# Optimization experiments

Measured on AMD Instinct MI355X. Metric: run time of the kernel, lower is better.

The kernel has to match this reference:

```python
import jax, jax.numpy as jnp
import numpy as np

B, S, DIM = 2, 1024, 1024
E, K, INTER = 16, 2, 512
SHARED_INTER = 2 * INTER  # n_shared_experts * moe_inter_dim
ROUTE_SCALE = 1.0


def setup_inputs() -> dict:
    key = jax.random.key(0)
    ks = jax.random.split(key, 8)
    init = lambda k, shape: jax.random.normal(k, shape, dtype=jnp.float32) * 0.02
    return {
        "x": jax.random.normal(ks[0], (B, S, DIM), dtype=jnp.float32),
        "gate_w": init(ks[1], (E, DIM)),
        "w1": init(ks[2], (E, INTER, DIM)),
        "w2": init(ks[3], (E, DIM, INTER)),
        "w3": init(ks[4], (E, INTER, DIM)),
        "sw1": init(ks[5], (SHARED_INTER, DIM)),
        "sw2": init(ks[6], (DIM, SHARED_INTER)),
        "sw3": init(ks[7], (SHARED_INTER, DIM)),
    }


def reference(x, gate_w, w1, w2, w3, sw1, sw2, sw3):
    b, s, d = x.shape
    xt = x.reshape(-1, d)            # [T, D] flattened tokens
    T = xt.shape[0]

    # Gate: sigmoid scores, top-k experts, normalize selected weights
    scores = jax.nn.sigmoid(xt @ gate_w.T)           # [T, E]
    topv, topi = jax.lax.top_k(scores, K)            # [T, K]
    weights = topv / jnp.sum(topv, axis=-1, keepdims=True) * ROUTE_SCALE

    # Per-token dense combine weights over experts: gate[t, e]
    gate = jnp.zeros((T, E), xt.dtype).at[jnp.arange(T)[:, None], topi].add(weights)

    # Routed experts (SwiGLU), computed densely and combined with gate weights
    h = jax.nn.silu(jnp.einsum('td,eid->tei', xt, w1)) * jnp.einsum('td,eid->tei', xt, w3)
    expert_out = jnp.einsum('tei,edi->ted', h, w2)   # [T, E, D]
    y = jnp.einsum('ted,te->td', expert_out, gate)   # [T, D]

    # Shared expert (SwiGLU MLP over all tokens)
    z = (jax.nn.silu(xt @ sw1.T) * (xt @ sw3.T)) @ sw2.T

    return (y + z).reshape(b, s, d)
```

## Files before the change

kernel.cpp:

```cpp
#include <hip/hip_runtime.h>
#include <stdint.h>

typedef unsigned short u16;
typedef __bf16 bf16x8 __attribute__((ext_vector_type(8)));
typedef float f32x4 __attribute__((ext_vector_type(4)));
typedef unsigned short u16x8 __attribute__((ext_vector_type(8)));

#define TTOK 2048
#define DIMSZ 1024
#define NROUT 16
#define INTERSZ 512
#define BK 128
#define CHK 16

__device__ __forceinline__ u16 f2bf(float f) {
    unsigned int u = __builtin_bit_cast(unsigned int, f);
    unsigned int r = u + 0x7FFFu + ((u >> 16) & 1u);
    return (u16)(r >> 16);
}

__device__ __forceinline__ void gl2lds16(const void* g, void* l) {
    __builtin_amdgcn_global_load_lds(
        (const __attribute__((address_space(1))) void*)(uintptr_t)g,
        (__attribute__((address_space(3))) void*)(uintptr_t)l,
        16, 0, 0);
}

#define NF4A (NROUT * INTERSZ * DIMSZ / 4)
#define NF4B (DIMSZ * DIMSZ / 4)
#define CASTA_BLKS 1024
#define CAST_BLKS 1152
__global__ __launch_bounds__(256) void prep(
    const float* __restrict__ w1, const float* __restrict__ sw1,
    const float* __restrict__ w3, const float* __restrict__ sw3,
    const float* __restrict__ w2, const float* __restrict__ sw2,
    u16* __restrict__ W1b, u16* __restrict__ W3b, u16* __restrict__ W2b,
    const float* __restrict__ x, const float* __restrict__ gw,
    int* __restrict__ topi, float2* __restrict__ topw,
    u16* __restrict__ Xbf) {
    const int r = blockIdx.y;
    const int tid = threadIdx.x;
    if (r < 3) {
        if (blockIdx.x >= CAST_BLKS) return;
        const float* a; const float* b; u16* d;
        if (r == 0)      { a = w1; b = sw1; d = W1b; }
        else if (r == 1) { a = w3; b = sw3; d = W3b; }
        else             { a = w2; b = sw2; d = W2b; }
        const float4* src = (blockIdx.x < CASTA_BLKS)
                            ? (const float4*)a
                            : (const float4*)b - (size_t)CASTA_BLKS * 2048;
        ushort4* dst = (ushort4*)d;
        const size_t gbase = (size_t)blockIdx.x * 2048;
        float4 v[8];
        #pragma unroll
        for (int k = 0; k < 8; ++k)
            v[k] = src[gbase + k * 256 + tid];
        #pragma unroll
        for (int k = 0; k < 8; ++k) {
            ushort4 o;
            o.x = f2bf(v[k].x); o.y = f2bf(v[k].y);
            o.z = f2bf(v[k].z); o.w = f2bf(v[k].w);
            dst[gbase + k * 256 + tid] = o;
        }
        return;
    }
    const int t = blockIdx.x;
    const int wave = tid >> 6, lane = tid & 63;
    const int d0 = tid * 4;
    float4 xv = *(const float4*)(x + (size_t)t * DIMSZ + d0);
    ushort4 o;
    o.x = f2bf(xv.x); o.y = f2bf(xv.y); o.z = f2bf(xv.z); o.w = f2bf(xv.w);
    *(ushort4*)&Xbf[(size_t)t * DIMSZ + d0] = o;

    float acc[16];
    #pragma unroll
    for (int e = 0; e < 16; ++e) {
        float4 g = *(const float4*)(gw + e * DIMSZ + d0);
        acc[e] = xv.x * g.x + xv.y * g.y + xv.z * g.z + xv.w * g.w;
    }
    #pragma unroll
    for (int off = 32; off > 0; off >>= 1) {
        #pragma unroll
        for (int e = 0; e < 16; ++e) acc[e] += __shfl_xor(acc[e], off);
    }
    __shared__ float part[4][16];
    __shared__ float sfin[16];
    if (lane < 16) part[wave][lane] = acc[lane];
    __syncthreads();
    if (wave == 0 && lane < 16) {
        float s = part[0][lane] + part[1][lane] + part[2][lane] + part[3][lane];
        sfin[lane] = 1.f / (1.f + expf(-s));
    }
    __syncthreads();
    if (tid == 0) {
        int i0 = 0; float v0 = sfin[0];
        #pragma unroll
        for (int e = 1; e < 16; ++e) { float v = sfin[e]; if (v > v0) { v0 = v; i0 = e; } }
        int i1 = -1; float v1 = -1e30f;
        #pragma unroll
        for (int e = 0; e < 16; ++e) { float v = sfin[e]; if (e != i0 && v > v1) { v1 = v; i1 = e; } }
        float inv = 1.f / (v0 + v1);
        topi[t] = i0 | (i1 << 8);
        topw[t] = make_float2(v0 * inv, v1 * inv);
    }
}

__global__ __launch_bounds__(256) void route_kernel(
    const int* __restrict__ topi, const float2* __restrict__ topw,
    int* __restrict__ counts, int* __restrict__ tokidx, float* __restrict__ tokw) {
    const int e = blockIdx.x;
    const int tid = threadIdx.x;
    int p[8]; int m[8]; int cnt = 0;
    #pragma unroll
    for (int j = 0; j < 8; ++j) {
        int t = tid * 8 + j;
        p[j] = topi[t];
        m[j] = ((p[j] & 255) == e) || ((p[j] >> 8) == e) ? 1 : 0;
        cnt += m[j];
    }
    const int lane = tid & 63, wave = tid >> 6;
    int v = cnt;
    #pragma unroll
    for (int off = 1; off < 64; off <<= 1) {
        int u = __shfl_up(v, off);
        if (lane >= off) v += u;
    }
    __shared__ int wsum[4];
    if (lane == 63) wsum[wave] = v;
    __syncthreads();
    int wbase = 0;
    #pragma unroll
    for (int w = 0; w < 4; ++w) wbase += (w < wave) ? wsum[w] : 0;
    int base = wbase + v - cnt;
    #pragma unroll
    for (int j = 0; j < 8; ++j) {
        if (m[j]) {
            int t = tid * 8 + j;
            float2 w2 = topw[t];
            tokidx[e * TTOK + base] = t;
            tokw[e * TTOK + base] = ((p[j] & 255) == e) ? w2.x : w2.y;
            ++base;
        }
    }
    if (tid == 0) counts[e] = wsum[0] + wsum[1] + wsum[2] + wsum[3];
}

__global__ __launch_bounds__(256) void gemm1s(
    const u16* __restrict__ Xbf, const u16* __restrict__ W1b,
    const u16* __restrict__ W3b, const int* __restrict__ counts,
    const int* __restrict__ tokidx, const float* __restrict__ tokw,
    u16* __restrict__ Hc, u16* __restrict__ Hs) {
    const int e = blockIdx.z;
    const int cnt = (e < NROUT) ? counts[e] : TTOK;
    const int m0 = blockIdx.y * 64;
    if (m0 >= cnt) return;
    const int n0 = blockIdx.x * 64;
    __shared__ u16 As[64 * BK], B1s[64 * BK], B3s[64 * BK];
    const u16* B1 = W1b + ((size_t)e * INTERSZ + n0) * DIMSZ;
    const u16* B3 = W3b + ((size_t)e * INTERSZ + n0) * DIMSZ;
    const int tid = threadIdx.x;

    int row[4], cgs[4]; size_t arow[4];
    #pragma unroll
    for (int i = 0; i < 4; ++i) {
        int c = tid + i * 256;
        row[i] = c >> 4;
        cgs[i] = ((c & 15) ^ (row[i] & 7)) * 8;
        int slot = m0 + row[i];
        int g;
        if (e < NROUT) g = (slot < cnt) ? tokidx[e * TTOK + slot] : 0;
        else           g = slot;
        arow[i] = (size_t)g * DIMSZ;
    }
    f32x4 acc1[2][2] = {}; f32x4 acc3[2][2] = {};
    const int wave = tid >> 6, lane = tid & 63;
    const int wm = (wave >> 1) * 32, wn = (wave & 1) * 32;
    const int lr = lane & 15, lq = lane >> 4;

    for (int kt = 0; kt < DIMSZ / BK; ++kt) {
        const int k0 = kt * BK;
        #pragma unroll
        for (int i = 0; i < 4; ++i) {
            int c = tid + i * 256;
            gl2lds16(Xbf + arow[i] + k0 + cgs[i], &As[c * 8]);
            size_t boff = (size_t)row[i] * DIMSZ + k0 + cgs[i];
            gl2lds16(B1 + boff, &B1s[c * 8]);
            gl2lds16(B3 + boff, &B3s[c * 8]);
        }
        __syncthreads();
        #pragma unroll
        for (int ks = 0; ks < 4; ++ks) {
            bf16x8 af[2], b1f[2], b3f[2];
            const int g = ks * 4 + lq;
            #pragma unroll
            for (int mt = 0; mt < 2; ++mt) {
                int m = wm + mt * 16 + lr;
                af[mt] = *(const bf16x8*)&As[(m * CHK + (g ^ (m & 7))) * 8];
            }
            #pragma unroll
            for (int nt = 0; nt < 2; ++nt) {
                int n = wn + nt * 16 + lr;
                int ch = (n * CHK + (g ^ (n & 7))) * 8;
                b1f[nt] = *(const bf16x8*)&B1s[ch];
                b3f[nt] = *(const bf16x8*)&B3s[ch];
            }
            #pragma unroll
            for (int mt = 0; mt < 2; ++mt) {
                #pragma unroll
                for (int nt = 0; nt < 2; ++nt) {
                    acc1[mt][nt] = __builtin_amdgcn_mfma_f32_16x16x32_bf16(af[mt], b1f[nt], acc1[mt][nt], 0, 0, 0);
                    acc3[mt][nt] = __builtin_amdgcn_mfma_f32_16x16x32_bf16(af[mt], b3f[nt], acc3[mt][nt], 0, 0, 0);
                }
            }
        }
        __syncthreads();
    }
    #pragma unroll
    for (int mt = 0; mt < 2; ++mt) {
        #pragma unroll
        for (int nt = 0; nt < 2; ++nt) {
            #pragma unroll
            for (int r = 0; r < 4; ++r) {
                int m = wm + mt * 16 + lq * 4 + r;
                int n = wn + nt * 16 + lr;
                int slot = m0 + m;
                bool valid = slot < cnt;
                float h1 = acc1[mt][nt][r], h3 = acc3[mt][nt][r];
                float hv = 0.f;
                if (valid) {
                    float tw = (e < NROUT) ? tokw[e * TTOK + slot] : 1.0f;
                    hv = h1 / (1.f + __expf(-h1)) * h3 * tw;
                }
                if (e < NROUT)
                    Hc[((size_t)e * TTOK + slot) * INTERSZ + n0 + n] = f2bf(hv);
                else
                    Hs[(size_t)slot * DIMSZ + (e - NROUT) * INTERSZ + n0 + n] = f2bf(hv);
            }
        }
    }
}

__global__ __launch_bounds__(256) void gemm2rt(
    const u16* __restrict__ Hc, const u16* __restrict__ W2b,
    const int* __restrict__ counts, const int* __restrict__ tokidx,
    const int* __restrict__ topi,
    float* __restrict__ bufA, float* __restrict__ bufB) {
    const int e = blockIdx.z;
    const int cnt = counts[e];
    const int m0 = blockIdx.y * 64;
    if (m0 >= cnt) return;
    const int n0 = blockIdx.x * 64;
    __shared__ u16 As[64 * BK], Bs[64 * BK];
    const u16* A0 = Hc + ((size_t)e * TTOK + m0) * INTERSZ;
    const u16* B0 = W2b + ((size_t)e * DIMSZ + n0) * INTERSZ;
    const int tid = threadIdx.x;
    const int wave = tid >> 6, lane = tid & 63;
    const int wm = (wave >> 1) * 32, wn = (wave & 1) * 32;
    const int lr = lane & 15, lq = lane >> 4;

    int row[4], cgs[4];
    #pragma unroll
    for (int i = 0; i < 4; ++i) {
        int c = tid + i * 256;
        row[i] = c >> 4;
        cgs[i] = ((c & 15) ^ (row[i] & 7)) * 8;
    }

    f32x4 acc[2][2] = {};
    for (int kt = 0; kt < INTERSZ / BK; ++kt) {
        const int k0 = kt * BK;
        #pragma unroll
        for (int i = 0; i < 4; ++i) {
            int c = tid + i * 256;
            gl2lds16(A0 + (size_t)row[i] * INTERSZ + k0 + cgs[i], &As[c * 8]);
            gl2lds16(B0 + (size_t)row[i] * INTERSZ + k0 + cgs[i], &Bs[c * 8]);
        }
        __syncthreads();
        #pragma unroll
        for (int ks = 0; ks < 4; ++ks) {
            bf16x8 af[2], bfr[2];
            const int g = ks * 4 + lq;
            #pragma unroll
            for (int mt = 0; mt < 2; ++mt) {
                int m = wm + mt * 16 + lr;
                af[mt] = *(const bf16x8*)&As[(m * CHK + (g ^ (m & 7))) * 8];
            }
            #pragma unroll
            for (int nt = 0; nt < 2; ++nt) {
                int n = wn + nt * 16 + lr;
                bfr[nt] = *(const bf16x8*)&Bs[(n * CHK + (g ^ (n & 7))) * 8];
            }
            #pragma unroll
            for (int mt = 0; mt < 2; ++mt) {
                #pragma unroll
                for (int nt = 0; nt < 2; ++nt) {
                    acc[mt][nt] = __builtin_amdgcn_mfma_f32_16x16x32_bf16(af[mt], bfr[nt], acc[mt][nt], 0, 0, 0);
                }
            }
        }
        __syncthreads();
    }
    #pragma unroll
    for (int mt = 0; mt < 2; ++mt) {
        #pragma unroll
        for (int r = 0; r < 4; ++r) {
            int m = wm + mt * 16 + lq * 4 + r;
            int slot = m0 + m;
            if (slot < cnt) {
                int t = tokidx[e * TTOK + slot];
                float* db = ((topi[t] & 255) == e) ? bufA : bufB;
                #pragma unroll
                for (int nt = 0; nt < 2; ++nt) {
                    int n = wn + nt * 16 + lr;
                    db[(size_t)t * DIMSZ + n0 + n] = acc[mt][nt][r];
                }
            }
        }
    }
}

__global__ __launch_bounds__(256) void gemm2sh(
    const u16* __restrict__ Hs, const u16* __restrict__ W2sb,
    const float* __restrict__ bufA, const float* __restrict__ bufB,
    float* __restrict__ out) {
    const int m0 = blockIdx.y * 64;
    const int n0 = blockIdx.x * 64;
    __shared__ u16 As[64 * BK], Bs[64 * BK];
    const u16* A0 = Hs + (size_t)m0 * DIMSZ;
    const u16* B0 = W2sb + (size_t)n0 * DIMSZ;
    const int tid = threadIdx.x;
    const int wave = tid >> 6, lane = tid & 63;
    const int wm = (wave >> 1) * 32, wn = (wave & 1) * 32;
    const int lr = lane & 15, lq = lane >> 4;

    int row[4], cgs[4];
    #pragma unroll
    for (int i = 0; i < 4; ++i) {
        int c = tid + i * 256;
        row[i] = c >> 4;
        cgs[i] = ((c & 15) ^ (row[i] & 7)) * 8;
    }

    f32x4 acc[2][2] = {};
    for (int kt = 0; kt < DIMSZ / BK; ++kt) {
        const int k0 = kt * BK;
        #pragma unroll
        for (int i = 0; i < 4; ++i) {
            int c = tid + i * 256;
            gl2lds16(A0 + (size_t)row[i] * DIMSZ + k0 + cgs[i], &As[c * 8]);
            gl2lds16(B0 + (size_t)row[i] * DIMSZ + k0 + cgs[i], &Bs[c * 8]);
        }
        __syncthreads();
        #pragma unroll
        for (int ks = 0; ks < 4; ++ks) {
            bf16x8 af[2], bfr[2];
            const int g = ks * 4 + lq;
            #pragma unroll
            for (int mt = 0; mt < 2; ++mt) {
                int m = wm + mt * 16 + lr;
                af[mt] = *(const bf16x8*)&As[(m * CHK + (g ^ (m & 7))) * 8];
            }
            #pragma unroll
            for (int nt = 0; nt < 2; ++nt) {
                int n = wn + nt * 16 + lr;
                bfr[nt] = *(const bf16x8*)&Bs[(n * CHK + (g ^ (n & 7))) * 8];
            }
            #pragma unroll
            for (int mt = 0; mt < 2; ++mt) {
                #pragma unroll
                for (int nt = 0; nt < 2; ++nt) {
                    acc[mt][nt] = __builtin_amdgcn_mfma_f32_16x16x32_bf16(af[mt], bfr[nt], acc[mt][nt], 0, 0, 0);
                }
            }
        }
        __syncthreads();
    }
    #pragma unroll
    for (int mt = 0; mt < 2; ++mt) {
        #pragma unroll
        for (int r = 0; r < 4; ++r) {
            int t = m0 + wm + mt * 16 + lq * 4 + r;
            #pragma unroll
            for (int nt = 0; nt < 2; ++nt) {
                int n = wn + nt * 16 + lr;
                size_t idx = (size_t)t * DIMSZ + n0 + n;
                out[idx] = acc[mt][nt][r] + bufA[idx] + bufB[idx];
            }
        }
    }
}

extern "C" void kernel_launch(void* const* d_in, const int* in_sizes, int n_in,
                              void* d_out, int out_size, void* d_ws, size_t ws_size,
                              hipStream_t stream) {
    const float* x      = (const float*)d_in[0];
    const float* gate_w = (const float*)d_in[1];
    const float* w1     = (const float*)d_in[2];
    const float* w2     = (const float*)d_in[3];
    const float* w3     = (const float*)d_in[4];
    const float* sw1    = (const float*)d_in[5];
    const float* sw2    = (const float*)d_in[6];
    const float* sw3    = (const float*)d_in[7];
    float* out = (float*)d_out;

    char* ws = (char*)d_ws;
    const size_t SZ_W   = (size_t)(NROUT + 2) * INTERSZ * DIMSZ * 2;
    const size_t SZ_XBF = (size_t)TTOK * DIMSZ * 2;
    u16*   W1b    = (u16*)(ws);
    u16*   W3b    = (u16*)(ws + SZ_W);
    u16*   W2all  = (u16*)(ws + 2 * SZ_W);
    u16*   Xbf    = (u16*)(ws + 3 * SZ_W);
    char*  route  = ws + 3 * SZ_W + SZ_XBF;
    int*   counts = (int*)route;
    int*   topi   = (int*)(route + 256);
    float2* topw  = (float2*)(route + 256 + TTOK * 4);
    int*   tokidx = (int*)(route + 256 + TTOK * 12);
    float* tokw   = (float*)(route + 256 + TTOK * 12 + 16 * TTOK * 4);
    char*  hbuf   = route + 256 + TTOK * 12 + 2 * (size_t)16 * TTOK * 4;
    u16*   Hc     = (u16*)hbuf;
    u16*   Hs     = (u16*)(hbuf + (size_t)NROUT * TTOK * INTERSZ * 2);
    char*  bufs   = hbuf + (size_t)NROUT * TTOK * INTERSZ * 2 + (size_t)TTOK * DIMSZ * 2;
    float* bufA   = (float*)bufs;
    float* bufB   = (float*)(bufs + (size_t)TTOK * DIMSZ * 4);
    u16*   W2sb   = W2all + (size_t)NROUT * DIMSZ * INTERSZ;

    prep<<<dim3(2048, 4), 256, 0, stream>>>(
        w1, sw1, w3, sw3, w2, sw2, W1b, W3b, W2all,
        x, gate_w, topi, topw, Xbf);
    route_kernel<<<NROUT, 256, 0, stream>>>(topi, topw, counts, tokidx, tokw);
    gemm1s<<<dim3(INTERSZ / 64, TTOK / 64, NROUT + 2), 256, 0, stream>>>(
        Xbf, W1b, W3b, counts, tokidx, tokw, Hc, Hs);
    gemm2rt<<<dim3(DIMSZ / 64, TTOK / 64, NROUT), 256, 0, stream>>>(
        Hc, W2all, counts, tokidx, topi, bufA, bufB);
    gemm2sh<<<dim3(DIMSZ / 64, TTOK / 64), 256, 0, stream>>>(
        Hs, W2sb, bufA, bufB, out);
}
```

Baseline: 230.8 us.

## Double-buffer LDS tiles in all GEMMs with BK 64 and split prep kernel

All three GEMM kernels now use BK=64 with two LDS buffers. The next K-tile is fetched by direct global-to-LDS loads while the current tile runs through MFMA, and a single wait plus barrier per iteration replaces the two syncthreads. s_setprio is raised during the MFMA section. The combined prep kernel is split into a weight-cast kernel and a gate/X-cast kernel, which removes the idle blocks of the old 2D grid. The risks are more loop iterations and barriers, and dependence on the loads in flight covering the compute of each iteration.

```diff
diff --git a/kernel.cpp b/kernel.cpp
--- a/kernel.cpp
+++ b/kernel.cpp
@@ -10,8 +10,8 @@
 #define DIMSZ 1024
 #define NROUT 16
 #define INTERSZ 512
-#define BK 128
-#define CHK 16
+#define BK 64
+#define CHK 8
 
 __device__ __forceinline__ u16 f2bf(float f) {
     unsigned int u = __builtin_bit_cast(unsigned int, f);
@@ -27,43 +27,41 @@
 }
 
 #define NF4A (NROUT * INTERSZ * DIMSZ / 4)
-#define NF4B (DIMSZ * DIMSZ / 4)
 #define CASTA_BLKS 1024
-#define CAST_BLKS 1152
-__global__ __launch_bounds__(256) void prep(
+__global__ __launch_bounds__(256) void prep_cast(
     const float* __restrict__ w1, const float* __restrict__ sw1,
     const float* __restrict__ w3, const float* __restrict__ sw3,
     const float* __restrict__ w2, const float* __restrict__ sw2,
-    u16* __restrict__ W1b, u16* __restrict__ W3b, u16* __restrict__ W2b,
+    u16* __restrict__ W1b, u16* __restrict__ W3b, u16* __restrict__ W2b) {
+    const int r = blockIdx.y;
+    const int tid = threadIdx.x;
+    const float* a; const float* b; u16* d;
+    if (r == 0)      { a = w1; b = sw1; d = W1b; }
+    else if (r == 1) { a = w3; b = sw3; d = W3b; }
+    else             { a = w2; b = sw2; d = W2b; }
+    const float4* src = (blockIdx.x < CASTA_BLKS)
+                        ? (const float4*)a
+                        : (const float4*)b - (size_t)CASTA_BLKS * 2048;
+    ushort4* dst = (ushort4*)d;
+    const size_t gbase = (size_t)blockIdx.x * 2048;
+    float4 v[8];
+    #pragma unroll
+    for (int k = 0; k < 8; ++k)
+        v[k] = src[gbase + k * 256 + tid];
+    #pragma unroll
+    for (int k = 0; k < 8; ++k) {
+        ushort4 o;
+        o.x = f2bf(v[k].x); o.y = f2bf(v[k].y);
+        o.z = f2bf(v[k].z); o.w = f2bf(v[k].w);
+        dst[gbase + k * 256 + tid] = o;
+    }
+}
+
+__global__ __launch_bounds__(256) void prep_gate(
     const float* __restrict__ x, const float* __restrict__ gw,
     int* __restrict__ topi, float2* __restrict__ topw,
     u16* __restrict__ Xbf) {
-    const int r = blockIdx.y;
-    const int tid = threadIdx.x;
-    if (r < 3) {
-        if (blockIdx.x >= CAST_BLKS) return;
-        const float* a; const float* b; u16* d;
-        if (r == 0)      { a = w1; b = sw1; d = W1b; }
-        else if (r == 1) { a = w3; b = sw3; d = W3b; }
-        else             { a = w2; b = sw2; d = W2b; }
-        const float4* src = (blockIdx.x < CASTA_BLKS)
-                            ? (const float4*)a
-                            : (const float4*)b - (size_t)CASTA_BLKS * 2048;
-        ushort4* dst = (ushort4*)d;
-        const size_t gbase = (size_t)blockIdx.x * 2048;
-        float4 v[8];
-        #pragma unroll
-        for (int k = 0; k < 8; ++k)
-            v[k] = src[gbase + k * 256 + tid];
-        #pragma unroll
-        for (int k = 0; k < 8; ++k) {
-            ushort4 o;
-            o.x = f2bf(v[k].x); o.y = f2bf(v[k].y);
-            o.z = f2bf(v[k].z); o.w = f2bf(v[k].w);
-            dst[gbase + k * 256 + tid] = o;
-        }
-        return;
-    }
+    const int tid = threadIdx.x;
     const int t = blockIdx.x;
     const int wave = tid >> 6, lane = tid & 63;
     const int d0 = tid * 4;
@@ -155,17 +153,17 @@
     const int m0 = blockIdx.y * 64;
     if (m0 >= cnt) return;
     const int n0 = blockIdx.x * 64;
-    __shared__ u16 As[64 * BK], B1s[64 * BK], B3s[64 * BK];
+    __shared__ u16 As[2][64 * BK], B1s[2][64 * BK], B3s[2][64 * BK];
     const u16* B1 = W1b + ((size_t)e * INTERSZ + n0) * DIMSZ;
     const u16* B3 = W3b + ((size_t)e * INTERSZ + n0) * DIMSZ;
     const int tid = threadIdx.x;
 
-    int row[4], cgs[4]; size_t arow[4];
-    #pragma unroll
-    for (int i = 0; i < 4; ++i) {
+    int row[2], cgs[2]; size_t arow[2];
+    #pragma unroll
+    for (int i = 0; i < 2; ++i) {
         int c = tid + i * 256;
-        row[i] = c >> 4;
-        cgs[i] = ((c & 15) ^ (row[i] & 7)) * 8;
+        row[i] = c >> 3;
+        cgs[i] = ((c & 7) ^ (row[i] & 7)) * 8;
         int slot = m0 + row[i];
         int g;
         if (e < NROUT) g = (slot < cnt) ? tokidx[e * TTOK + slot] : 0;
@@ -176,33 +174,43 @@
     const int wave = tid >> 6, lane = tid & 63;
     const int wm = (wave >> 1) * 32, wn = (wave & 1) * 32;
     const int lr = lane & 15, lq = lane >> 4;
-
-    for (int kt = 0; kt < DIMSZ / BK; ++kt) {
-        const int k0 = kt * BK;
-        #pragma unroll
-        for (int i = 0; i < 4; ++i) {
-            int c = tid + i * 256;
-            gl2lds16(Xbf + arow[i] + k0 + cgs[i], &As[c * 8]);
-            size_t boff = (size_t)row[i] * DIMSZ + k0 + cgs[i];
-            gl2lds16(B1 + boff, &B1s[c * 8]);
-            gl2lds16(B3 + boff, &B3s[c * 8]);
-        }
-        __syncthreads();
-        #pragma unroll
-        for (int ks = 0; ks < 4; ++ks) {
+    const int NKT = DIMSZ / BK;
+
+#define STG1(kt, h) { \
+    const int k0_ = (kt) * BK; \
+    _Pragma("unroll") \
+    for (int i = 0; i < 2; ++i) { \
+        int c = tid + i * 256; \
+        gl2lds16(Xbf + arow[i] + k0_ + cgs[i], &As[h][c * 8]); \
+        size_t boff = (size_t)row[i] * DIMSZ + k0_ + cgs[i]; \
+        gl2lds16(B1 + boff, &B1s[h][c * 8]); \
+        gl2lds16(B3 + boff, &B3s[h][c * 8]); \
+    } }
+
+    STG1(0, 0);
+    asm volatile("s_waitcnt vmcnt(0)" ::: "memory");
+    __builtin_amdgcn_s_barrier();
+
+    #pragma unroll 2
+    for (int kt = 0; kt < NKT; ++kt) {
+        const int cur = kt & 1;
+        if (kt + 1 < NKT) STG1(kt + 1, cur ^ 1);
+        __builtin_amdgcn_s_setprio(1);
+        #pragma unroll
+        for (int ks = 0; ks < 2; ++ks) {
             bf16x8 af[2], b1f[2], b3f[2];
             const int g = ks * 4 + lq;
             #pragma unroll
             for (int mt = 0; mt < 2; ++mt) {
                 int m = wm + mt * 16 + lr;
-                af[mt] = *(const bf16x8*)&As[(m * CHK + (g ^ (m & 7))) * 8];
+                af[mt] = *(const bf16x8*)&As[cur][(m * CHK + (g ^ (m & 7))) * 8];
             }
             #pragma unroll
             for (int nt = 0; nt < 2; ++nt) {
                 int n = wn + nt * 16 + lr;
                 int ch = (n * CHK + (g ^ (n & 7))) * 8;
-                b1f[nt] = *(const bf16x8*)&B1s[ch];
-                b3f[nt] = *(const bf16x8*)&B3s[ch];
+                b1f[nt] = *(const bf16x8*)&B1s[cur][ch];
+                b3f[nt] = *(const bf16x8*)&B3s[cur][ch];
             }
             #pragma unroll
             for (int mt = 0; mt < 2; ++mt) {
@@ -213,8 +221,11 @@
                 }
             }
         }
-        __syncthreads();
-    }
+        __builtin_amdgcn_s_setprio(0);
+        asm volatile("s_waitcnt vmcnt(0)" ::: "memory");
+        __builtin_amdgcn_s_barrier();
+    }
+#undef STG1
     #pragma unroll
     for (int mt = 0; mt < 2; ++mt) {
         #pragma unroll
@@ -250,7 +261,7 @@
     const int m0 = blockIdx.y * 64;
     if (m0 >= cnt) return;
     const int n0 = blockIdx.x * 64;
-    __shared__ u16 As[64 * BK], Bs[64 * BK];
+    __shared__ u16 As[2][64 * BK], Bs[2][64 * BK];
     const u16* A0 = Hc + ((size_t)e * TTOK + m0) * INTERSZ;
     const u16* B0 = W2b + ((size_t)e * DIMSZ + n0) * INTERSZ;
     const int tid = threadIdx.x;
@@ -258,37 +269,47 @@
     const int wm = (wave >> 1) * 32, wn = (wave & 1) * 32;
     const int lr = lane & 15, lq = lane >> 4;
 
-    int row[4], cgs[4];
-    #pragma unroll
-    for (int i = 0; i < 4; ++i) {
+    int row[2], cgs[2];
+    #pragma unroll
+    for (int i = 0; i < 2; ++i) {
         int c = tid + i * 256;
-        row[i] = c >> 4;
-        cgs[i] = ((c & 15) ^ (row[i] & 7)) * 8;
-    }
-
+        row[i] = c >> 3;
+        cgs[i] = ((c & 7) ^ (row[i] & 7)) * 8;
+    }
     f32x4 acc[2][2] = {};
-    for (int kt = 0; kt < INTERSZ / BK; ++kt) {
-        const int k0 = kt * BK;
-        #pragma unroll
-        for (int i = 0; i < 4; ++i) {
-            int c = tid + i * 256;
-            gl2lds16(A0 + (size_t)row[i] * INTERSZ + k0 + cgs[i], &As[c * 8]);
-            gl2lds16(B0 + (size_t)row[i] * INTERSZ + k0 + cgs[i], &Bs[c * 8]);
-        }
-        __syncthreads();
-        #pragma unroll
-        for (int ks = 0; ks < 4; ++ks) {
+    const int NKT = INTERSZ / BK;
+
+#define STG2(kt, h) { \
+    const int k0_ = (kt) * BK; \
+    _Pragma("unroll") \
+    for (int i = 0; i < 2; ++i) { \
+        int c = tid + i * 256; \
+        gl2lds16(A0 + (size_t)row[i] * INTERSZ + k0_ + cgs[i], &As[h][c * 8]); \
+        gl2lds16(B0 + (size_t)row[i] * INTERSZ + k0_ + cgs[i], &Bs[h][c * 8]); \
+    } }
+
+    STG2(0, 0);
+    asm volatile("s_waitcnt vmcnt(0)" ::: "memory");
+    __builtin_amdgcn_s_barrier();
+
+    #pragma unroll 2
+    for (int kt = 0; kt < NKT; ++kt) {
+        const int cur = kt & 1;
+        if (kt + 1 < NKT) STG2(kt + 1, cur ^ 1);
+        __builtin_amdgcn_s_setprio(1);
+        #pragma unroll
+        for (int ks = 0; ks < 2; ++ks) {
             bf16x8 af[2], bfr[2];
             const int g = ks * 4 + lq;
             #pragma unroll
             for (int mt = 0; mt < 2; ++mt) {
                 int m = wm + mt * 16 + lr;
-                af[mt] = *(const bf16x8*)&As[(m * CHK + (g ^ (m & 7))) * 8];
+                af[mt] = *(const bf16x8*)&As[cur][(m * CHK + (g ^ (m & 7))) * 8];
             }
             #pragma unroll
             for (int nt = 0; nt < 2; ++nt) {
                 int n = wn + nt * 16 + lr;
-                bfr[nt] = *(const bf16x8*)&Bs[(n * CHK + (g ^ (n & 7))) * 8];
+                bfr[nt] = *(const bf16x8*)&Bs[cur][(n * CHK + (g ^ (n & 7))) * 8];
             }
             #pragma unroll
             for (int mt = 0; mt < 2; ++mt) {
@@ -298,8 +319,11 @@
                 }
             }
         }
-        __syncthreads();
-    }
+        __builtin_amdgcn_s_setprio(0);
+        asm volatile("s_waitcnt vmcnt(0)" ::: "memory");
+        __builtin_amdgcn_s_barrier();
+    }
+#undef STG2
     #pragma unroll
     for (int mt = 0; mt < 2; ++mt) {
         #pragma unroll
@@ -325,7 +349,7 @@
     float* __restrict__ out) {
     const int m0 = blockIdx.y * 64;
     const int n0 = blockIdx.x * 64;
-    __shared__ u16 As[64 * BK], Bs[64 * BK];
+    __shared__ u16 As[2][64 * BK], Bs[2][64 * BK];
     const u16* A0 = Hs + (size_t)m0 * DIMSZ;
     const u16* B0 = W2sb + (size_t)n0 * DIMSZ;
     const int tid = threadIdx.x;
@@ -333,37 +357,47 @@
     const int wm = (wave >> 1) * 32, wn = (wave & 1) * 32;
     const int lr = lane & 15, lq = lane >> 4;
 
-    int row[4], cgs[4];
-    #pragma unroll
-    for (int i = 0; i < 4; ++i) {
+    int row[2], cgs[2];
+    #pragma unroll
+    for (int i = 0; i < 2; ++i) {
         int c = tid + i * 256;
-        row[i] = c >> 4;
-        cgs[i] = ((c & 15) ^ (row[i] & 7)) * 8;
-    }
-
+        row[i] = c >> 3;
+        cgs[i] = ((c & 7) ^ (row[i] & 7)) * 8;
+    }
     f32x4 acc[2][2] = {};
-    for (int kt = 0; kt < DIMSZ / BK; ++kt) {
-        const int k0 = kt * BK;
-        #pragma unroll
-        for (int i = 0; i < 4; ++i) {
-            int c = tid + i * 256;
-            gl2lds16(A0 + (size_t)row[i] * DIMSZ + k0 + cgs[i], &As[c * 8]);
-            gl2lds16(B0 + (size_t)row[i] * DIMSZ + k0 + cgs[i], &Bs[c * 8]);
-        }
-        __syncthreads();
-        #pragma unroll
-        for (int ks = 0; ks < 4; ++ks) {
+    const int NKT = DIMSZ / BK;
+
+#define STG3(kt, h) { \
+    const int k0_ = (kt) * BK; \
+    _Pragma("unroll") \
+    for (int i = 0; i < 2; ++i) { \
+        int c = tid + i * 256; \
+        gl2lds16(A0 + (size_t)row[i] * DIMSZ + k0_ + cgs[i], &As[h][c * 8]); \
+        gl2lds16(B0 + (size_t)row[i] * DIMSZ + k0_ + cgs[i], &Bs[h][c * 8]); \
+    } }
+
+    STG3(0, 0);
+    asm volatile("s_waitcnt vmcnt(0)" ::: "memory");
+    __builtin_amdgcn_s_barrier();
+
+    #pragma unroll 2
+    for (int kt = 0; kt < NKT; ++kt) {
+        const int cur = kt & 1;
+        if (kt + 1 < NKT) STG3(kt + 1, cur ^ 1);
+        __builtin_amdgcn_s_setprio(1);
+        #pragma unroll
+        for (int ks = 0; ks < 2; ++ks) {
             bf16x8 af[2], bfr[2];
             const int g = ks * 4 + lq;
             #pragma unroll
             for (int mt = 0; mt < 2; ++mt) {
                 int m = wm + mt * 16 + lr;
-                af[mt] = *(const bf16x8*)&As[(m * CHK + (g ^ (m & 7))) * 8];
+                af[mt] = *(const bf16x8*)&As[cur][(m * CHK + (g ^ (m & 7))) * 8];
             }
             #pragma unroll
             for (int nt = 0; nt < 2; ++nt) {
                 int n = wn + nt * 16 + lr;
-                bfr[nt] = *(const bf16x8*)&Bs[(n * CHK + (g ^ (n & 7))) * 8];
+                bfr[nt] = *(const bf16x8*)&Bs[cur][(n * CHK + (g ^ (n & 7))) * 8];
             }
             #pragma unroll
             for (int mt = 0; mt < 2; ++mt) {
@@ -373,8 +407,11 @@
                 }
             }
         }
-        __syncthreads();
-    }
+        __builtin_amdgcn_s_setprio(0);
+        asm volatile("s_waitcnt vmcnt(0)" ::: "memory");
+        __builtin_amdgcn_s_barrier();
+    }
+#undef STG3
     #pragma unroll
     for (int mt = 0; mt < 2; ++mt) {
         #pragma unroll
@@ -424,9 +461,9 @@
     float* bufB   = (float*)(bufs + (size_t)TTOK * DIMSZ * 4);
     u16*   W2sb   = W2all + (size_t)NROUT * DIMSZ * INTERSZ;
 
-    prep<<<dim3(2048, 4), 256, 0, stream>>>(
-        w1, sw1, w3, sw3, w2, sw2, W1b, W3b, W2all,
-        x, gate_w, topi, topw, Xbf);
+    prep_cast<<<dim3(1152, 3), 256, 0, stream>>>(
+        w1, sw1, w3, sw3, w2, sw2, W1b, W3b, W2all);
+    prep_gate<<<dim3(2048), 256, 0, stream>>>(x, gate_w, topi, topw, Xbf);
     route_kernel<<<NROUT, 256, 0, stream>>>(topi, topw, counts, tokidx, tokw);
     gemm1s<<<dim3(INTERSZ / 64, TTOK / 64, NROUT + 2), 256, 0, stream>>>(
         Xbf, W1b, W3b, counts, tokidx, tokw, Hc, Hs);
```

Result: no change. 235.3 us (+1.9%).

## Fuse w2 bf16 cast into routed GEMM2 and keep weight tile resident in LDS

Applied to the files above, without the earlier changes.

Drops the separate fp32-to-bf16 cast of the routed w2 weights in the prep kernel. Each gemm2rt block now loads its 64x512 fp32 slice of w2 once, converts it and stores it swizzled in LDS. It then loops over every 64-token chunk routed to that expert. This removes one full write and re-read of the bf16 w2 copy and the repeated B-tile loads per M tile. In exchange the grid shrinks to 256 blocks that each run a serial token loop, and the 64KB B tile in LDS reduces occupancy.

```diff
diff --git a/kernel.cpp b/kernel.cpp
--- a/kernel.cpp
+++ b/kernel.cpp
@@ -19,6 +19,12 @@
     return (u16)(r >> 16);
 }
 
+__device__ __forceinline__ ushort4 cvt4(float4 a) {
+    ushort4 o;
+    o.x = f2bf(a.x); o.y = f2bf(a.y); o.z = f2bf(a.z); o.w = f2bf(a.w);
+    return o;
+}
+
 __device__ __forceinline__ void gl2lds16(const void* g, void* l) {
     __builtin_amdgcn_global_load_lds(
         (const __attribute__((address_space(1))) void*)(uintptr_t)g,
@@ -27,50 +33,49 @@
 }
 
 #define NF4A (NROUT * INTERSZ * DIMSZ / 4)
-#define NF4B (DIMSZ * DIMSZ / 4)
 #define CASTA_BLKS 1024
 #define CAST_BLKS 1152
+#define SW2_BLKS 128
 __global__ __launch_bounds__(256) void prep(
     const float* __restrict__ w1, const float* __restrict__ sw1,
     const float* __restrict__ w3, const float* __restrict__ sw3,
-    const float* __restrict__ w2, const float* __restrict__ sw2,
-    u16* __restrict__ W1b, u16* __restrict__ W3b, u16* __restrict__ W2b,
+    const float* __restrict__ sw2,
+    u16* __restrict__ W1b, u16* __restrict__ W3b, u16* __restrict__ W2sb,
     const float* __restrict__ x, const float* __restrict__ gw,
     int* __restrict__ topi, float2* __restrict__ topw,
     u16* __restrict__ Xbf) {
     const int r = blockIdx.y;
     const int tid = threadIdx.x;
     if (r < 3) {
-        if (blockIdx.x >= CAST_BLKS) return;
-        const float* a; const float* b; u16* d;
-        if (r == 0)      { a = w1; b = sw1; d = W1b; }
-        else if (r == 1) { a = w3; b = sw3; d = W3b; }
-        else             { a = w2; b = sw2; d = W2b; }
-        const float4* src = (blockIdx.x < CASTA_BLKS)
-                            ? (const float4*)a
-                            : (const float4*)b - (size_t)CASTA_BLKS * 2048;
-        ushort4* dst = (ushort4*)d;
+        const float4* src; ushort4* dst;
+        if (r < 2) {
+            if (blockIdx.x >= CAST_BLKS) return;
+            const float* a = r ? w3 : w1;
+            const float* b = r ? sw3 : sw1;
+            dst = (ushort4*)(r ? W3b : W1b);
+            src = (blockIdx.x < CASTA_BLKS)
+                  ? (const float4*)a
+                  : (const float4*)b - (size_t)CASTA_BLKS * 2048;
+        } else {
+            if (blockIdx.x >= SW2_BLKS) return;
+            src = (const float4*)sw2;
+            dst = (ushort4*)W2sb;
+        }
         const size_t gbase = (size_t)blockIdx.x * 2048;
         float4 v[8];
         #pragma unroll
         for (int k = 0; k < 8; ++k)
             v[k] = src[gbase + k * 256 + tid];
         #pragma unroll
-        for (int k = 0; k < 8; ++k) {
-            ushort4 o;
-            o.x = f2bf(v[k].x); o.y = f2bf(v[k].y);
-            o.z = f2bf(v[k].z); o.w = f2bf(v[k].w);
-            dst[gbase + k * 256 + tid] = o;
-        }
+        for (int k = 0; k < 8; ++k)
+            dst[gbase + k * 256 + tid] = cvt4(v[k]);
         return;
     }
     const int t = blockIdx.x;
     const int wave = tid >> 6, lane = tid & 63;
     const int d0 = tid * 4;
     float4 xv = *(const float4*)(x + (size_t)t * DIMSZ + d0);
-    ushort4 o;
-    o.x = f2bf(xv.x); o.y = f2bf(xv.y); o.z = f2bf(xv.z); o.w = f2bf(xv.w);
-    *(ushort4*)&Xbf[(size_t)t * DIMSZ + d0] = o;
+    *(ushort4*)&Xbf[(size_t)t * DIMSZ + d0] = cvt4(xv);
 
     float acc[16];
     #pragma unroll
@@ -241,23 +246,38 @@
 }
 
 __global__ __launch_bounds__(256) void gemm2rt(
-    const u16* __restrict__ Hc, const u16* __restrict__ W2b,
+    const u16* __restrict__ Hc, const float* __restrict__ w2f,
     const int* __restrict__ counts, const int* __restrict__ tokidx,
     const int* __restrict__ topi,
     float* __restrict__ bufA, float* __restrict__ bufB) {
-    const int e = blockIdx.z;
+    const int e = blockIdx.y;
+    const int n0 = blockIdx.x * 64;
     const int cnt = counts[e];
-    const int m0 = blockIdx.y * 64;
-    if (m0 >= cnt) return;
-    const int n0 = blockIdx.x * 64;
-    __shared__ u16 As[64 * BK], Bs[64 * BK];
-    const u16* A0 = Hc + ((size_t)e * TTOK + m0) * INTERSZ;
-    const u16* B0 = W2b + ((size_t)e * DIMSZ + n0) * INTERSZ;
     const int tid = threadIdx.x;
+    __shared__ u16 Bs[64 * INTERSZ];
+    __shared__ u16 As[64 * BK];
+
+    const float4* B0 = (const float4*)(w2f + ((size_t)e * DIMSZ + n0) * INTERSZ);
+    #pragma unroll
+    for (int it2 = 0; it2 < 4; ++it2) {
+        float4 v[8];
+        #pragma unroll
+        for (int k = 0; k < 8; ++k)
+            v[k] = B0[(it2 * 8 + k) * 256 + tid];
+        #pragma unroll
+        for (int k = 0; k < 8; ++k) {
+            int q = (it2 * 8 + k) * 256 + tid;
+            int brow = q >> 7;
+            int c = (q & 127) >> 1;
+            int h = q & 1;
+            *(ushort4*)&Bs[((brow << 6) + (c ^ (brow & 7))) * 8 + h * 4] = cvt4(v[k]);
+        }
+    }
+    __syncthreads();
+
     const int wave = tid >> 6, lane = tid & 63;
     const int wm = (wave >> 1) * 32, wn = (wave & 1) * 32;
     const int lr = lane & 15, lq = lane >> 4;
-
     int row[4], cgs[4];
     #pragma unroll
     for (int i = 0; i < 4; ++i) {
@@ -266,53 +286,55 @@
         cgs[i] = ((c & 15) ^ (row[i] & 7)) * 8;
     }
 
-    f32x4 acc[2][2] = {};
-    for (int kt = 0; kt < INTERSZ / BK; ++kt) {
-        const int k0 = kt * BK;
-        #pragma unroll
-        for (int i = 0; i < 4; ++i) {
-            int c = tid + i * 256;
-            gl2lds16(A0 + (size_t)row[i] * INTERSZ + k0 + cgs[i], &As[c * 8]);
-            gl2lds16(B0 + (size_t)row[i] * INTERSZ + k0 + cgs[i], &Bs[c * 8]);
-        }
-        __syncthreads();
-        #pragma unroll
-        for (int ks = 0; ks < 4; ++ks) {
-            bf16x8 af[2], bfr[2];
-            const int g = ks * 4 + lq;
-            #pragma unroll
-            for (int mt = 0; mt < 2; ++mt) {
-                int m = wm + mt * 16 + lr;
-                af[mt] = *(const bf16x8*)&As[(m * CHK + (g ^ (m & 7))) * 8];
-            }
-            #pragma unroll
-            for (int nt = 0; nt < 2; ++nt) {
-                int n = wn + nt * 16 + lr;
-                bfr[nt] = *(const bf16x8*)&Bs[(n * CHK + (g ^ (n & 7))) * 8];
-            }
-            #pragma unroll
-            for (int mt = 0; mt < 2; ++mt) {
+    for (int m0 = 0; m0 < cnt; m0 += 64) {
+        const u16* A0 = Hc + ((size_t)e * TTOK + m0) * INTERSZ;
+        f32x4 acc[2][2] = {};
+        for (int kt = 0; kt < INTERSZ / BK; ++kt) {
+            const int k0 = kt * BK;
+            #pragma unroll
+            for (int i = 0; i < 4; ++i) {
+                int c = tid + i * 256;
+                gl2lds16(A0 + (size_t)row[i] * INTERSZ + k0 + cgs[i], &As[c * 8]);
+            }
+            __syncthreads();
+            #pragma unroll
+            for (int ks = 0; ks < 4; ++ks) {
+                bf16x8 af[2], bfr[2];
+                const int g = ks * 4 + lq;
                 #pragma unroll
-                for (int nt = 0; nt < 2; ++nt) {
-                    acc[mt][nt] = __builtin_amdgcn_mfma_f32_16x16x32_bf16(af[mt], bfr[nt], acc[mt][nt], 0, 0, 0);
-                }
-            }
-        }
-        __syncthreads();
-    }
-    #pragma unroll
-    for (int mt = 0; mt < 2; ++mt) {
-        #pragma unroll
-        for (int r = 0; r < 4; ++r) {
-            int m = wm + mt * 16 + lq * 4 + r;
-            int slot = m0 + m;
-            if (slot < cnt) {
-                int t = tokidx[e * TTOK + slot];
-                float* db = ((topi[t] & 255) == e) ? bufA : bufB;
+                for (int mt = 0; mt < 2; ++mt) {
+                    int m = wm + mt * 16 + lr;
+                    af[mt] = *(const bf16x8*)&As[(m * CHK + (g ^ (m & 7))) * 8];
+                }
                 #pragma unroll
                 for (int nt = 0; nt < 2; ++nt) {
                     int n = wn + nt * 16 + lr;
-                    db[(size_t)t * DIMSZ + n0 + n] = acc[mt][nt][r];
+                    bfr[nt] = *(const bf16x8*)&Bs[(n * 64 + kt * CHK + (g ^ (n & 7))) * 8];
+                }
+                #pragma unroll
+                for (int mt = 0; mt < 2; ++mt) {
+                    #pragma unroll
+                    for (int nt = 0; nt < 2; ++nt) {
+                        acc[mt][nt] = __builtin_amdgcn_mfma_f32_16x16x32_bf16(af[mt], bfr[nt], acc[mt][nt], 0, 0, 0);
+                    }
+                }
+            }
+            __syncthreads();
+        }
+        #pragma unroll
+        for (int mt = 0; mt < 2; ++mt) {
+            #pragma unroll
+            for (int r = 0; r < 4; ++r) {
+                int m = wm + mt * 16 + lq * 4 + r;
+                int slot = m0 + m;
+                if (slot < cnt) {
+                    int t = tokidx[e * TTOK + slot];
+                    float* db = ((topi[t] & 255) == e) ? bufA : bufB;
+                    #pragma unroll
+                    for (int nt = 0; nt < 2; ++nt) {
+                        int n = wn + nt * 16 + lr;
+                        db[(size_t)t * DIMSZ + n0 + n] = acc[mt][nt][r];
+                    }
                 }
             }
         }
@@ -425,13 +447,13 @@
     u16*   W2sb   = W2all + (size_t)NROUT * DIMSZ * INTERSZ;
 
     prep<<<dim3(2048, 4), 256, 0, stream>>>(
-        w1, sw1, w3, sw3, w2, sw2, W1b, W3b, W2all,
+        w1, sw1, w3, sw3, sw2, W1b, W3b, W2sb,
         x, gate_w, topi, topw, Xbf);
     route_kernel<<<NROUT, 256, 0, stream>>>(topi, topw, counts, tokidx, tokw);
     gemm1s<<<dim3(INTERSZ / 64, TTOK / 64, NROUT + 2), 256, 0, stream>>>(
         Xbf, W1b, W3b, counts, tokidx, tokw, Hc, Hs);
-    gemm2rt<<<dim3(DIMSZ / 64, TTOK / 64, NROUT), 256, 0, stream>>>(
-        Hc, W2all, counts, tokidx, topi, bufA, bufB);
+    gemm2rt<<<dim3(DIMSZ / 64, NROUT), 256, 0, stream>>>(
+        Hc, w2, counts, tokidx, topi, bufA, bufB);
     gemm2sh<<<dim3(DIMSZ / 64, TTOK / 64), 256, 0, stream>>>(
         Hs, W2sb, bufA, bufB, out);
 }
```

Result: slower. 239.0 us (+3.6%).
